# Performance work log

Hardware: AMD Instinct MI355X
Metric: run time of the kernel (lower is better)

Reference implementation:

```python
import jax, jax.numpy as jnp
import numpy as np
from jax import lax

# quantization bit widths (config)
IB, WB, RB, AB = 8, 4, 4, 8


def quantize(x, bw):
    """Signed fixed-point quantization to bw bits in [-1, 1) with STE."""
    scale = 2.0 ** (bw - 1)
    q = jnp.clip(jnp.round(x * scale), -scale, scale - 1) / scale
    return x + lax.stop_gradient(q - x)


def setup_inputs() -> dict:
    key = jax.random.key(0)
    k1, k2, k3, k4, k5 = jax.random.split(key, 5)
    B, T, I, H, O = 256, 1024, 64, 256, 16
    inputs = jax.random.normal(k1, (B, T, I), dtype=jnp.float32)
    # input kernel init: uniform(-1, 1)
    Wi = jax.random.uniform(k2, (H, I), dtype=jnp.float32, minval=-1.0, maxval=1.0)
    # recurrent kernel: orthogonal (geotorch parametrization); materialize via QR
    A = jax.random.normal(k3, (H, H), dtype=jnp.float32)
    Wr, _ = jnp.linalg.qr(A)
    Wr = Wr.astype(jnp.float32)
    Wo = jax.random.normal(k4, (O, H), dtype=jnp.float32) * 0.1
    b = jax.random.normal(k5, (H,), dtype=jnp.float32) * 0.01
    return {"inputs": inputs, "Wi": Wi, "Wr": Wr, "Wo": Wo, "b": b}


def reference(inputs, Wi, Wr, Wo, b):
    # quantize inputs (ib bits)
    x = quantize(inputs, IB)
    # quantized input projection, precomputed for all timesteps: [B,T,H]
    u = jnp.einsum("bti,hi->bth", x, quantize(Wi, WB))
    Wrq = quantize(Wr, RB)  # quantized orthogonal recurrent weight [H,H]
    B = inputs.shape[0]
    H = Wr.shape[0]
    h0 = jnp.zeros((B, H), dtype=inputs.dtype)

    def step(h, u_t):
        z = u_t + h @ Wrq.T                      # [B,H]
        m = jax.nn.relu(jnp.abs(z) + b)          # modrelu magnitude
        h_new = quantize(jnp.sign(z) * m, AB)    # quantized activation
        return h_new, None

    u_t = jnp.swapaxes(u, 0, 1)  # [T,B,H]
    h_last, _ = lax.scan(step, h0, u_t)
    # output head on last hidden state
    out = h_last @ quantize(Wo, WB).T  # [B,O]
    return out
```

## Files before the change

kernel.cpp:

```cpp
#include <hip/hip_runtime.h>


#define TSEQ 1024
#define IDIM 64
#define HDIM 256
#define ODIM 16
#define CHUNK 16
#define NCHUNK (TSEQ / CHUNK)

__device__ __forceinline__ int sdot4i8(int a, int b, int c) {
#if __has_builtin(__builtin_amdgcn_sdot4)
    return __builtin_amdgcn_sdot4(a, b, c, false);
#else
    int r = c;
    r += ((a << 24) >> 24) * ((b << 24) >> 24);
    r += ((a << 16) >> 24) * ((b << 16) >> 24);
    r += ((a << 8)  >> 24) * ((b << 8)  >> 24);
    r += (a >> 24) * (b >> 24);
    return r;
#endif
}

__device__ __forceinline__ int qpack4(float4 f, float s, float lo, float hi) {
    int a = (int)fminf(fmaxf(rintf(f.x * s), lo), hi);
    int b = (int)fminf(fmaxf(rintf(f.y * s), lo), hi);
    int c = (int)fminf(fmaxf(rintf(f.z * s), lo), hi);
    int d = (int)fminf(fmaxf(rintf(f.w * s), lo), hi);
    return (a & 255) | ((b & 255) << 8) | ((c & 255) << 16) | ((d & 255) << 24);
}

__device__ __forceinline__ int quad_reduce_add(int v) {
    v += __builtin_amdgcn_update_dpp(0, v, 0xB1, 0xF, 0xF, true);
    v += __builtin_amdgcn_update_dpp(0, v, 0x4E, 0xF, 0xF, true);
    return v;
}

__global__ __launch_bounds__(256, 1)
void qornn_kernel(const float* __restrict__ x, const float* __restrict__ Wi,
                  const float* __restrict__ Wr, const float* __restrict__ Wo,
                  const float* __restrict__ bias, float* __restrict__ out) {
    __shared__ alignas(16) int wstage[8192];
    __shared__ alignas(16) int xbuf[2][256];
    __shared__ alignas(16) int hbuf[2][64];

    const int tid = threadIdx.x;
    const int brow = blockIdx.x;
    const int w    = tid >> 6;
    const int l    = tid & 63;
    const int q    = l & 3;
    const int m16  = l >> 2;
    const int obase = w * 64 + m16 * 4;

    {
        const float4* wi4 = (const float4*)Wi;
        #pragma unroll
        for (int it = 0; it < 16; ++it) {
            int flat = it * 256 + tid;
            wstage[flat] = qpack4(wi4[flat], 8.0f, -8.0f, 7.0f);
        }
    }
    __syncthreads();
    int4 wiq[4];
    {
        const int4* p = (const int4*)wstage;
        #pragma unroll
        for (int i = 0; i < 4; ++i) wiq[i] = p[(obase + i) * 4 + q];
    }
    __syncthreads();

    int4 wr[16];
    {
        const float4* wr4 = (const float4*)Wr;
        #pragma unroll
        for (int it = 0; it < 32; ++it) {
            int flat = it * 256 + tid;
            wstage[flat] = qpack4(wr4[flat], 8.0f, -8.0f, 7.0f);
        }
        __syncthreads();
        if (obase < 128) {
            const int4* p = (const int4*)wstage;
            #pragma unroll
            for (int i = 0; i < 4; ++i)
                #pragma unroll
                for (int r = 0; r < 4; ++r)
                    wr[i * 4 + r] = p[(obase + i) * 16 + q * 4 + r];
        }
        __syncthreads();
        #pragma unroll
        for (int it = 0; it < 32; ++it) {
            int flat = it * 256 + tid;
            wstage[flat] = qpack4(wr4[8192 + flat], 8.0f, -8.0f, 7.0f);
        }
        __syncthreads();
        if (obase >= 128) {
            const int4* p = (const int4*)wstage;
            #pragma unroll
            for (int i = 0; i < 4; ++i)
                #pragma unroll
                for (int r = 0; r < 4; ++r)
                    wr[i * 4 + r] = p[(obase - 128 + i) * 16 + q * 4 + r];
        }
        __syncthreads();
    }

    {
        const float4* wo4 = (const float4*)Wo;
        #pragma unroll
        for (int it = 0; it < 4; ++it) {
            int flat = it * 256 + tid;
            wstage[flat] = qpack4(wo4[flat], 8.0f, -8.0f, 7.0f);
        }
    }

    const float4 bv4 = *(const float4*)(bias + obase);
    const float bvv[4] = {bv4.x, bv4.y, bv4.z, bv4.w};

    const float4* rowf4 = (const float4*)(x + (size_t)brow * (TSEQ * IDIM));
    {
        float4 xf = rowf4[tid];
        xbuf[0][tid] = qpack4(xf, 128.0f, -128.0f, 127.0f);
        if (tid < 64) hbuf[0][tid] = 0;
    }
    __syncthreads();

    for (int c = 0; c < NCHUNK; ++c) {
        float4 nf;
        if (c < NCHUNK - 1) nf = rowf4[(c + 1) * 256 + tid];
        const int xb = c & 1;
        const int* xbase = xbuf[xb];

        #pragma unroll
        for (int s = 0; s < CHUNK; ++s) {
            const int pb = s & 1;
            int4 hh[4];
            {
                const int4* hP = (const int4*)hbuf[pb];
                #pragma unroll
                for (int r = 0; r < 4; ++r) hh[r] = hP[q * 4 + r];
            }
            const int4 xx = ((const int4*)(xbase + s * 16))[q];

            int acc[4] = {0, 0, 0, 0};
            #pragma unroll
            for (int r = 0; r < 4; ++r) {
                #pragma unroll
                for (int i = 0; i < 4; ++i) {
                    const int4 wv = wr[i * 4 + r];
                    acc[i] = sdot4i8(hh[r].x, wv.x, acc[i]);
                    acc[i] = sdot4i8(hh[r].y, wv.y, acc[i]);
                    acc[i] = sdot4i8(hh[r].z, wv.z, acc[i]);
                    acc[i] = sdot4i8(hh[r].w, wv.w, acc[i]);
                }
            }
            #pragma unroll
            for (int i = 0; i < 4; ++i) {
                acc[i] = sdot4i8(xx.x, wiq[i].x, acc[i]);
                acc[i] = sdot4i8(xx.y, wiq[i].y, acc[i]);
                acc[i] = sdot4i8(xx.z, wiq[i].z, acc[i]);
                acc[i] = sdot4i8(xx.w, wiq[i].w, acc[i]);
            }

            int packed = 0;
            #pragma unroll
            for (int i = 0; i < 4; ++i) {
                const int z = quad_reduce_add(acc[i]);
                const float zf = (float)z;
                const float t1 = fmaf(fabsf(zf), 0.0009765625f, bvv[i]);
                const float t2 = fmaxf(t1, 0.0f);
                const float r  = rintf(t2 * 128.0f);
                const float rp = fminf(r, 127.0f);
                const float rn = fminf(r, 128.0f);
                int v = (z < 0) ? -(int)rn : (int)rp;
                v = (z == 0) ? 0 : v;
                packed |= (v & 255) << (8 * i);
            }
            if (q == 0) hbuf[pb ^ 1][w * 16 + m16] = packed;

            if (s == CHUNK - 1 && c < NCHUNK - 1) {
                xbuf[xb ^ 1][tid] = qpack4(nf, 128.0f, -128.0f, 127.0f);
            }
            __syncthreads();
        }
    }

    if (tid < ODIM) {
        const int4* wo = (const int4*)wstage;
        const int4* hl = (const int4*)hbuf[0];
        int a0 = 0, a1 = 0, a2 = 0, a3 = 0;
        #pragma unroll
        for (int i = 0; i < 16; ++i) {
            int4 w4 = wo[tid * 16 + i];
            int4 h4 = hl[i];
            a0 = sdot4i8(h4.x, w4.x, a0);
            a1 = sdot4i8(h4.y, w4.y, a1);
            a2 = sdot4i8(h4.z, w4.z, a2);
            a3 = sdot4i8(h4.w, w4.w, a3);
        }
        out[brow * ODIM + tid] = (float)((a0 + a1) + (a2 + a3)) * 0.0009765625f;
    }
}

extern "C" void kernel_launch(void* const* d_in, const int* in_sizes, int n_in,
                              void* d_out, int out_size, void* d_ws, size_t ws_size,
                              hipStream_t stream) {
    const float* x  = (const float*)d_in[0];
    const float* Wi = (const float*)d_in[1];
    const float* Wr = (const float*)d_in[2];
    const float* Wo = (const float*)d_in[3];
    const float* b  = (const float*)d_in[4];
    float* out = (float*)d_out;

    const int B = in_sizes[0] / (TSEQ * IDIM);
    qornn_kernel<<<B, HDIM, 0, stream>>>(x, Wi, Wr, Wo, b, out);
}
```

Baseline: 516.9 us.

## Preload quantized input row to LDS and pipeline the input projection per timestep

The whole quantized input sequence for a batch row now goes into LDS once, replacing the chunked double-buffered staging. The next timestep's input projection is computed alongside the current recurrent dot product, taking it off the serial critical path. The recurrent dot chain is split into two accumulators for more instruction-level parallelism. Each quad lane now finishes the activation for one hidden unit and writes a single byte, instead of one lane doing all four. In exchange LDS use rises to about 96KB, and the up-front load of the input row is serialized before the recurrence starts.

After: 423.1 us. 1.22x faster.

```diff
diff --git a/kernel.cpp b/kernel.cpp
--- a/kernel.cpp
+++ b/kernel.cpp
@@ -5,8 +5,6 @@
 #define IDIM 64
 #define HDIM 256
 #define ODIM 16
-#define CHUNK 16
-#define NCHUNK (TSEQ / CHUNK)
 
 __device__ __forceinline__ int sdot4i8(int a, int b, int c) {
 #if __has_builtin(__builtin_amdgcn_sdot4)
@@ -29,7 +27,7 @@
     return (a & 255) | ((b & 255) << 8) | ((c & 255) << 16) | ((d & 255) << 24);
 }
 
-__device__ __forceinline__ int quad_reduce_add(int v) {
+__device__ __forceinline__ int qsum(int v) {
     v += __builtin_amdgcn_update_dpp(0, v, 0xB1, 0xF, 0xF, true);
     v += __builtin_amdgcn_update_dpp(0, v, 0x4E, 0xF, 0xF, true);
     return v;
@@ -39,8 +37,8 @@
 void qornn_kernel(const float* __restrict__ x, const float* __restrict__ Wi,
                   const float* __restrict__ Wr, const float* __restrict__ Wo,
                   const float* __restrict__ bias, float* __restrict__ out) {
+    __shared__ alignas(16) int xlds[TSEQ * 16 + 16];
     __shared__ alignas(16) int wstage[8192];
-    __shared__ alignas(16) int xbuf[2][256];
     __shared__ alignas(16) int hbuf[2][64];
 
     const int tid = threadIdx.x;
@@ -112,75 +110,97 @@
         }
     }
 
-    const float4 bv4 = *(const float4*)(bias + obase);
-    const float bvv[4] = {bv4.x, bv4.y, bv4.z, bv4.w};
-
-    const float4* rowf4 = (const float4*)(x + (size_t)brow * (TSEQ * IDIM));
-    {
-        float4 xf = rowf4[tid];
-        xbuf[0][tid] = qpack4(xf, 128.0f, -128.0f, 127.0f);
-        if (tid < 64) hbuf[0][tid] = 0;
-    }
+    {
+        const float4* rowf4 = (const float4*)(x + (size_t)brow * (TSEQ * IDIM));
+        #pragma unroll 8
+        for (int it = 0; it < 64; ++it) {
+            int flat = it * 256 + tid;
+            xlds[flat] = qpack4(rowf4[flat], 128.0f, -128.0f, 127.0f);
+        }
+    }
+    if (tid < 64) hbuf[0][tid] = 0;
     __syncthreads();
 
-    for (int c = 0; c < NCHUNK; ++c) {
-        float4 nf;
-        if (c < NCHUNK - 1) nf = rowf4[(c + 1) * 256 + tid];
-        const int xb = c & 1;
-        const int* xbase = xbuf[xb];
-
-        #pragma unroll
-        for (int s = 0; s < CHUNK; ++s) {
-            const int pb = s & 1;
-            int4 hh[4];
-            {
-                const int4* hP = (const int4*)hbuf[pb];
-                #pragma unroll
-                for (int r = 0; r < 4; ++r) hh[r] = hP[q * 4 + r];
-            }
-            const int4 xx = ((const int4*)(xbase + s * 16))[q];
-
-            int acc[4] = {0, 0, 0, 0};
+    const float bv = bias[tid];
+    const bool qb0 = (q & 1) != 0;
+    const bool qb1 = (q & 2) != 0;
+
+    int u[4];
+    {
+        const int4 xx = ((const int4*)xlds)[q];
+        #pragma unroll
+        for (int i = 0; i < 4; ++i) {
+            int s = sdot4i8(xx.x, wiq[i].x, 0);
+            s = sdot4i8(xx.y, wiq[i].y, s);
+            s = sdot4i8(xx.z, wiq[i].z, s);
+            u[i] = sdot4i8(xx.w, wiq[i].w, s);
+        }
+    }
+
+    #pragma unroll 2
+    for (int t = 0; t < TSEQ; ++t) {
+        int4 hh[4];
+        {
+            const int4* hP = (const int4*)hbuf[t & 1];
             #pragma unroll
-            for (int r = 0; r < 4; ++r) {
-                #pragma unroll
-                for (int i = 0; i < 4; ++i) {
-                    const int4 wv = wr[i * 4 + r];
-                    acc[i] = sdot4i8(hh[r].x, wv.x, acc[i]);
-                    acc[i] = sdot4i8(hh[r].y, wv.y, acc[i]);
-                    acc[i] = sdot4i8(hh[r].z, wv.z, acc[i]);
-                    acc[i] = sdot4i8(hh[r].w, wv.w, acc[i]);
-                }
-            }
-            #pragma unroll
-            for (int i = 0; i < 4; ++i) {
-                acc[i] = sdot4i8(xx.x, wiq[i].x, acc[i]);
-                acc[i] = sdot4i8(xx.y, wiq[i].y, acc[i]);
-                acc[i] = sdot4i8(xx.z, wiq[i].z, acc[i]);
-                acc[i] = sdot4i8(xx.w, wiq[i].w, acc[i]);
-            }
-
-            int packed = 0;
-            #pragma unroll
-            for (int i = 0; i < 4; ++i) {
-                const int z = quad_reduce_add(acc[i]);
-                const float zf = (float)z;
-                const float t1 = fmaf(fabsf(zf), 0.0009765625f, bvv[i]);
-                const float t2 = fmaxf(t1, 0.0f);
-                const float r  = rintf(t2 * 128.0f);
-                const float rp = fminf(r, 127.0f);
-                const float rn = fminf(r, 128.0f);
-                int v = (z < 0) ? -(int)rn : (int)rp;
-                v = (z == 0) ? 0 : v;
-                packed |= (v & 255) << (8 * i);
-            }
-            if (q == 0) hbuf[pb ^ 1][w * 16 + m16] = packed;
-
-            if (s == CHUNK - 1 && c < NCHUNK - 1) {
-                xbuf[xb ^ 1][tid] = qpack4(nf, 128.0f, -128.0f, 127.0f);
-            }
-            __syncthreads();
-        }
+            for (int r = 0; r < 4; ++r) hh[r] = hP[q * 4 + r];
+        }
+        const int4 xn = ((const int4*)xlds)[(t + 1) * 4 + q];
+
+        int za[4], zb[4];
+        #pragma unroll
+        for (int i = 0; i < 4; ++i) {
+            int s0 = u[i];
+            s0 = sdot4i8(hh[0].x, wr[i * 4 + 0].x, s0);
+            s0 = sdot4i8(hh[0].y, wr[i * 4 + 0].y, s0);
+            s0 = sdot4i8(hh[0].z, wr[i * 4 + 0].z, s0);
+            s0 = sdot4i8(hh[0].w, wr[i * 4 + 0].w, s0);
+            s0 = sdot4i8(hh[1].x, wr[i * 4 + 1].x, s0);
+            s0 = sdot4i8(hh[1].y, wr[i * 4 + 1].y, s0);
+            s0 = sdot4i8(hh[1].z, wr[i * 4 + 1].z, s0);
+            s0 = sdot4i8(hh[1].w, wr[i * 4 + 1].w, s0);
+            int s1 = 0;
+            s1 = sdot4i8(hh[2].x, wr[i * 4 + 2].x, s1);
+            s1 = sdot4i8(hh[2].y, wr[i * 4 + 2].y, s1);
+            s1 = sdot4i8(hh[2].z, wr[i * 4 + 2].z, s1);
+            s1 = sdot4i8(hh[2].w, wr[i * 4 + 2].w, s1);
+            s1 = sdot4i8(hh[3].x, wr[i * 4 + 3].x, s1);
+            s1 = sdot4i8(hh[3].y, wr[i * 4 + 3].y, s1);
+            s1 = sdot4i8(hh[3].z, wr[i * 4 + 3].z, s1);
+            s1 = sdot4i8(hh[3].w, wr[i * 4 + 3].w, s1);
+            za[i] = s0; zb[i] = s1;
+        }
+        int un[4];
+        #pragma unroll
+        for (int i = 0; i < 4; ++i) {
+            int s = sdot4i8(xn.x, wiq[i].x, 0);
+            s = sdot4i8(xn.y, wiq[i].y, s);
+            s = sdot4i8(xn.z, wiq[i].z, s);
+            un[i] = sdot4i8(xn.w, wiq[i].w, s);
+        }
+
+        const int z0 = qsum(za[0] + zb[0]);
+        const int z1 = qsum(za[1] + zb[1]);
+        const int z2 = qsum(za[2] + zb[2]);
+        const int z3 = qsum(za[3] + zb[3]);
+        const int zlo = qb0 ? z1 : z0;
+        const int zhi = qb0 ? z3 : z2;
+        const int z   = qb1 ? zhi : zlo;
+
+        const float zf = (float)z;
+        const float t1 = fmaf(fabsf(zf), 0.0009765625f, bv);
+        const float t2 = fmaxf(t1, 0.0f);
+        const float r  = rintf(t2 * 128.0f);
+        const int vpos = (int)fminf(r, 127.0f);
+        const int vneg = -(int)fminf(r, 128.0f);
+        int hv = (z < 0) ? vneg : vpos;
+        hv = (z == 0) ? 0 : hv;
+
+        ((signed char*)hbuf[(t + 1) & 1])[tid] = (signed char)hv;
+
+        #pragma unroll
+        for (int i = 0; i < 4; ++i) u[i] = un[i];
+        __syncthreads();
     }
 
     if (tid < ODIM) {
```
